# Performance work log

Measured on AMD Instinct MI355X. Metric: run time of the kernel, lower is better.

The kernel has to match this reference:

```python
import jax, jax.numpy as jnp
import numpy as np
import math

NQ = 12          # num_qubits
DEPTH = 4        # circuit_depth
DIM = 2 ** NQ    # state_dim = 4096
B = 4096         # batch

# CNOT ladder: (i,i+1) plus wrap-around (n-1,0) when n>2 (as in _init_circuit_parameters)
CNOT_PAIRS = [(i, i + 1) for i in range(NQ - 1)] + ([(NQ - 1, 0)] if NQ > 2 else [])


def _rx(theta):
    c = jnp.cos(theta / 2).astype(jnp.complex64)
    s = jnp.sin(theta / 2).astype(jnp.complex64) * (-1j)
    return jnp.stack([jnp.stack([c, s]), jnp.stack([s, c])])


def _ry(phi):
    c = jnp.cos(phi / 2).astype(jnp.complex64)
    s = jnp.sin(phi / 2).astype(jnp.complex64)
    return jnp.stack([jnp.stack([c, -s]), jnp.stack([s, c])])


def _rz(lam):
    lamc = lam.astype(jnp.complex64)
    e0 = jnp.exp(-1j * lamc / 2)
    e1 = jnp.exp(1j * lamc / 2)
    z = jnp.zeros((), jnp.complex64)
    return jnp.stack([jnp.stack([e0, z]), jnp.stack([z, e1])])


def _apply_1q(state, gate, q):
    # state: [B] + [2]*NQ, qubit q lives on axis q+1 (kron order: qubit 0 most significant)
    ax = q + 1
    s = jnp.moveaxis(state, ax, -1)
    s = jnp.einsum('ab,...b->...a', gate, s)
    return jnp.moveaxis(s, -1, ax)


def _apply_cnot(state, control, target):
    # flip target bit on the control=1 half of the state vector
    ac, at = control + 1, target + 1
    s0 = jnp.take(state, jnp.array([0]), axis=ac)
    s1 = jnp.take(state, jnp.array([1]), axis=ac)
    s1 = jnp.flip(s1, axis=at)
    return jnp.concatenate([s0, s1], axis=ac)


def setup_inputs() -> dict:
    key = jax.random.key(0)
    k1, k2, k3, k4 = jax.random.split(key, 4)
    return {
        'input_data': jax.random.normal(k1, (B, DIM), dtype=jnp.float32),
        'angles_x': jax.random.normal(k2, (DEPTH, NQ), dtype=jnp.float32) * 0.5,
        'angles_y': jax.random.normal(k3, (DEPTH, NQ), dtype=jnp.float32) * 0.5,
        'angles_z': jax.random.normal(k4, (DEPTH, NQ), dtype=jnp.float32) * 0.5,
    }


def reference(input_data, angles_x, angles_y, angles_z):
    # --- amplitude encoding (faithful to quantum_weight_memory) ---
    w = jnp.abs(input_data[:, :DIM])                      # [B, D]
    D = w.shape[1]
    s = jnp.sum(w, axis=1, keepdims=True)
    wn = jnp.where(s > 1e-8, w / jnp.sqrt(jnp.maximum(s, 1e-8)),
                   jnp.full_like(w, 1.0 / math.sqrt(D)))
    state = jnp.zeros((w.shape[0], DIM), jnp.complex64).at[:, 0].set(1.0)
    state = state.at[:, :D].set(wn.astype(jnp.complex64))
    norm = jnp.sqrt(jnp.sum(jnp.abs(state) ** 2, axis=1, keepdims=True))
    state = jnp.where(norm > 1e-8, state / jnp.maximum(norm, 1e-8), state)

    # --- parametrized circuit, applied as local state-vector updates ---
    state = state.reshape((state.shape[0],) + (2,) * NQ)
    for layer in range(DEPTH):
        for q in range(NQ):
            state = _apply_1q(state, _rx(angles_x[layer, q]), q)
            state = _apply_1q(state, _ry(angles_y[layer, q]), q)
            state = _apply_1q(state, _rz(angles_z[layer, q]), q)
        for c, t in CNOT_PAIRS:
            state = _apply_cnot(state, c, t)
    state = state.reshape(-1, DIM)

    # --- measurement ---
    probs = jnp.abs(state) ** 2
    return jnp.sqrt(probs[:, :DIM])
```

## Files before the change

### kernel.cpp

```cpp
#include <hip/hip_runtime.h>
#include <math.h>

#define DIM 4096

typedef _Float16 v8h __attribute__((ext_vector_type(8)));
typedef float v4f __attribute__((ext_vector_type(4)));

__device__ __forceinline__ int pinv(int s) {
  int p = __popc(s) & 1;
  int d = s ^ (p ? 0xC00 : 0);
  d ^= d >> 1; d ^= d >> 2; d ^= d >> 4; d ^= d >> 8;
  return d & 4095;
}
constexpr int pinv_c(int s) {
  int p = __builtin_popcount(s) & 1;
  int d = s ^ (p ? 0xC00 : 0);
  d ^= d >> 1; d ^= d >> 2; d ^= d >> 4; d ^= d >> 8;
  return d & 4095;
}

__device__ __forceinline__ int swz4(int row) {
  return (((row >> 1) ^ (row >> 5)) & 3) << 4;
}

constexpr int l0d(int d) {
  int row = (d & 15) * 16 + ((d >> 4) & 15);
  int f2 = ((row >> 1) ^ (row >> 5)) & 3;
  return (row << 6) ^ ((((d >> 8) & 15)) << 1) ^ (f2 << 4);
}

constexpr int DR1 = l0d(pinv_c(1 << 8));
constexpr int DR2 = l0d(pinv_c(2 << 8));
constexpr int DR3 = l0d(pinv_c(3 << 8));

template <int PASS>
__device__ __forceinline__ void do_pass(const char* src, char* dst,
                                        const v8h* __restrict__ Af, int mat, int t) {
  const int lane = t & 63, wv = t >> 6;
  const int m = lane & 15, q = lane >> 4, qb = q & 1, pm = q >> 1;
  const v8h b_re = Af[(mat * 2 + 0) * 64 + lane];
  const v8h b_im = Af[(mat * 2 + 1) * 64 + lane];
  int abase = 0;
  if constexpr (PASS == 2) {
    abase = l0d(pinv((q << 10) | (wv << 6) | m));
  }
#pragma unroll
  for (int tt = 0; tt < 4; ++tt) {
    const int t4 = wv * 4 + tt;
    const int row = t4 * 16 + m;
    const int sz = swz4(row);
    v8h a;
    if constexpr (PASS == 0) {
      a = *(const v8h*)(src + (((row << 6) + pm * 32 + qb * 16) ^ sz));
    } else {
      const int ad = ((row << 6) + qb * 32 + pm * 8) ^ sz;
      const uint2 lo = *(const uint2*)(src + ad);
      const uint2 hi = *(const uint2*)(src + (ad ^ 16));
      a = __builtin_bit_cast(v8h, make_uint4(lo.x, lo.y, hi.x, hi.y));
    }
    const v4f cre = __builtin_amdgcn_mfma_f32_16x16x32_f16(a, b_re, (v4f){0.f, 0.f, 0.f, 0.f}, 0, 0, 0);
    const v4f cim = __builtin_amdgcn_mfma_f32_16x16x32_f16(a, b_im, (v4f){0.f, 0.f, 0.f, 0.f}, 0, 0, 0);
    if constexpr (PASS < 2) {
      const int wrow = m * 16 + t4;
      v8h w;
#pragma unroll
      for (int r = 0; r < 4; ++r) {
        w[r] = (_Float16)cre[r];
        w[4 + r] = (_Float16)cim[r];
      }
      *(v8h*)(dst + (((wrow << 6) + q * 16) ^ swz4(wrow))) = w;
    } else {
      const int ab = abase ^ l0d(pinv_c(tt << 4));
      *(_Float16*)(dst + ab) = (_Float16)cre[0];
      *(_Float16*)(dst + (ab ^ DR1)) = (_Float16)cre[1];
      *(_Float16*)(dst + (ab ^ DR2)) = (_Float16)cre[2];
      *(_Float16*)(dst + (ab ^ DR3)) = (_Float16)cre[3];
      *(_Float16*)(dst + (ab ^ 32)) = (_Float16)cim[0];
      *(_Float16*)(dst + (ab ^ (DR1 ^ 32))) = (_Float16)cim[1];
      *(_Float16*)(dst + (ab ^ (DR2 ^ 32))) = (_Float16)cim[2];
      *(_Float16*)(dst + (ab ^ (DR3 ^ 32))) = (_Float16)cim[3];
    }
  }
}

__global__ void make_gates2(const float* __restrict__ ax, const float* __restrict__ ay,
                            const float* __restrict__ az, _Float16* __restrict__ Aw) {
  __shared__ float g4[48][4];
  const int id = threadIdx.x;
  if (id < 48) {
    float th = 0.5f * ax[id], ph = 0.5f * ay[id], lm = 0.5f * az[id];
    float c = cosf(th), s = sinf(th);
    float cy = cosf(ph), sy = sinf(ph);
    float cl = cosf(lm), sl = sinf(lm);
    float m00r = cy * c, m00i = sy * s;
    float m01r = -sy * c, m01i = -cy * s;
    g4[id][0] = cl * m00r + sl * m00i;
    g4[id][1] = cl * m00i - sl * m00r;
    g4[id][2] = cl * m01r + sl * m01i;
    g4[id][3] = cl * m01i - sl * m01r;
  }
  __syncthreads();
  const int mat = id >> 6, lane = id & 63;
  const int m = lane & 15, q = lane >> 4;
  const int layer = mat / 3, pass = mat % 3, qbase = pass * 4;
#pragma unroll
  for (int j = 0; j < 8; ++j) {
    const int k = q * 8 + j, kk = k & 15;
    float cr = 1.f, ci = 0.f;
#pragma unroll
    for (int bp = 3; bp >= 0; --bp) {
      const int qq = qbase + (3 - bp);
      const int ib = (m >> bp) & 1, kb = (kk >> bp) & 1;
      const float* gg = g4[layer * 12 + qq];
      float er, ei;
      if (ib == 0 && kb == 0) { er = gg[0]; ei = gg[1]; }
      else if (ib == 0 && kb == 1) { er = gg[2]; ei = gg[3]; }
      else if (ib == 1 && kb == 0) { er = -gg[2]; ei = gg[3]; }
      else { er = gg[0]; ei = -gg[1]; }
      const float nr = cr * er - ci * ei, ni = cr * ei + ci * er;
      cr = nr; ci = ni;
    }
    const float reval = (k < 16) ? cr : -ci;
    const float imval = (k < 16) ? ci : cr;
    Aw[((mat * 2 + 0) * 64 + lane) * 8 + j] = (_Float16)reval;
    Aw[((mat * 2 + 1) * 64 + lane) * 8 + j] = (_Float16)imval;
  }
}

__global__ __launch_bounds__(256, 4) void qsim3(const float* __restrict__ x,
                                                const v8h* __restrict__ Af,
                                                float* __restrict__ out) {
  __shared__ __align__(16) char buf[2][16384];
  const int t = threadIdx.x;
  const int b = blockIdx.x;
  const float* xb = x + (size_t)b * DIM;

  float w[16];
  float sw = 0.f, sw2 = 0.f;
#pragma unroll
  for (int j = 0; j < 16; ++j) {
    float a = fabsf(xb[t + (j << 8)]);
    w[j] = a; sw += a; sw2 += a * a;
  }
#pragma unroll
  for (int off = 32; off; off >>= 1) {
    sw += __shfl_down(sw, off, 64);
    sw2 += __shfl_down(sw2, off, 64);
  }
  float* red = (float*)buf[1];
  if ((t & 63) == 0) { red[t >> 6] = sw; red[4 + (t >> 6)] = sw2; }
  __syncthreads();
  sw = (red[0] + red[1]) + (red[2] + red[3]);
  sw2 = (red[4] + red[5]) + (red[6] + red[7]);

  float sc = 0.f;
  const bool ok = (sw > 1e-8f);
  if (ok) {
    float wnscale = rsqrtf(fmaxf(sw, 1e-8f));
    float norm = sqrtf(sw2 / sw);
    sc = ((norm > 1e-8f) ? (wnscale / fmaxf(norm, 1e-8f)) : wnscale) * 64.0f;
  }
  {
    const int row = ((t & 15) << 4) | (t >> 4);
    const int rb = (row << 6) ^ swz4(row);
    v8h h0, h1, z;
#pragma unroll
    for (int j = 0; j < 8; ++j) {
      h0[j] = (_Float16)(ok ? w[j] * sc : 1.0f);
      h1[j] = (_Float16)(ok ? w[8 + j] * sc : 1.0f);
      z[j] = (_Float16)0.f;
    }
    *(v8h*)(buf[0] + (rb ^ 0)) = h0;
    *(v8h*)(buf[0] + (rb ^ 16)) = h1;
    *(v8h*)(buf[0] + (rb ^ 32)) = z;
    *(v8h*)(buf[0] + (rb ^ 48)) = z;
  }
  __syncthreads();

  char* s = buf[0];
  char* d = buf[1];
#pragma unroll 1
  for (int l = 0; l < 4; ++l) {
    do_pass<0>(s, d, Af, l * 3 + 0, t);
    __syncthreads();
    do_pass<1>(d, s, Af, l * 3 + 1, t);
    __syncthreads();
    do_pass<2>(s, d, Af, l * 3 + 2, t);
    __syncthreads();
    char* tmp = s; s = d; d = tmp;
  }

  float* ob = out + (size_t)b * DIM;
  {
    const int row = ((t & 15) << 4) | (t >> 4);
    const int rb = (row << 6) ^ swz4(row);
    const v8h r0 = *(const v8h*)(s + (rb ^ 0));
    const v8h r1 = *(const v8h*)(s + (rb ^ 16));
    const v8h i0 = *(const v8h*)(s + (rb ^ 32));
    const v8h i1 = *(const v8h*)(s + (rb ^ 48));
#pragma unroll
    for (int j = 0; j < 8; ++j) {
      float re = (float)r0[j], im = (float)i0[j];
      ob[(j << 8) | t] = sqrtf(re * re + im * im) * 0.015625f;
      float re2 = (float)r1[j], im2 = (float)i1[j];
      ob[((j + 8) << 8) | t] = sqrtf(re2 * re2 + im2 * im2) * 0.015625f;
    }
  }
}

extern "C" void kernel_launch(void* const* d_in, const int* in_sizes, int n_in,
                              void* d_out, int out_size, void* d_ws, size_t ws_size,
                              hipStream_t stream) {
  const float* x = (const float*)d_in[0];
  const float* ax = (const float*)d_in[1];
  const float* ay = (const float*)d_in[2];
  const float* az = (const float*)d_in[3];
  _Float16* Aw = (_Float16*)d_ws;
  make_gates2<<<1, 768, 0, stream>>>(ax, ay, az, Aw);
  qsim3<<<4096, 256, 0, stream>>>(x, (const v8h*)Aw, (float*)d_out);
}
```

Measured before the change: 176.2 us.

## Replace scattered CNOT permutation stores with vectorized stores and fold permutation into loads

Pass 2 used to write eight scattered 2-byte halves per MFMA so that the CNOT-ladder permutation landed in the store addresses. It now writes two 8-byte vectors in plain order. The permutation is absorbed later, by Gray-code-style indexing plus byte perms in the next layer's first pass and in the final output read. Pass 1 loads become single 16-byte reads rearranged with permlane32_swap, and the LDS swizzle gains an extra bit to reduce bank conflicts. The aim is fewer LDS transactions and less address arithmetic, at the cost of more complex index logic with a higher risk of subtle permutation errors.

```diff
diff --git a/kernel.cpp b/kernel.cpp
--- a/kernel.cpp
+++ b/kernel.cpp
@@ -4,81 +4,76 @@
 #define DIM 4096
 
 typedef _Float16 v8h __attribute__((ext_vector_type(8)));
+typedef _Float16 v4h __attribute__((ext_vector_type(4)));
 typedef float v4f __attribute__((ext_vector_type(4)));
-
-__device__ __forceinline__ int pinv(int s) {
-  int p = __popc(s) & 1;
-  int d = s ^ (p ? 0xC00 : 0);
-  d ^= d >> 1; d ^= d >> 2; d ^= d >> 4; d ^= d >> 8;
-  return d & 4095;
-}
-constexpr int pinv_c(int s) {
-  int p = __builtin_popcount(s) & 1;
-  int d = s ^ (p ? 0xC00 : 0);
-  d ^= d >> 1; d ^= d >> 2; d ^= d >> 4; d ^= d >> 8;
-  return d & 4095;
-}
-
-__device__ __forceinline__ int swz4(int row) {
-  return (((row >> 1) ^ (row >> 5)) & 3) << 4;
-}
-
-constexpr int l0d(int d) {
-  int row = (d & 15) * 16 + ((d >> 4) & 15);
-  int f2 = ((row >> 1) ^ (row >> 5)) & 3;
-  return (row << 6) ^ ((((d >> 8) & 15)) << 1) ^ (f2 << 4);
-}
-
-constexpr int DR1 = l0d(pinv_c(1 << 8));
-constexpr int DR2 = l0d(pinv_c(2 << 8));
-constexpr int DR3 = l0d(pinv_c(3 << 8));
-
-template <int PASS>
-__device__ __forceinline__ void do_pass(const char* src, char* dst,
+typedef unsigned int v2u __attribute__((ext_vector_type(2)));
+
+__device__ __forceinline__ int adr(int row, int off) {
+  return ((row << 6) | off) ^ ((((row >> 1) ^ (row >> 5)) & 3) << 4)
+                            ^ (((row >> 4) & 1) << 6);
+}
+
+
+template <int PASS, bool FOLD>
+__device__ __forceinline__ void do_pass(const char* __restrict__ src, char* __restrict__ dst,
                                         const v8h* __restrict__ Af, int mat, int t) {
   const int lane = t & 63, wv = t >> 6;
-  const int m = lane & 15, q = lane >> 4, qb = q & 1, pm = q >> 1;
+  const int m = lane & 15, q = lane >> 4;
+  const int qb = q & 1, pm = q >> 1;
   const v8h b_re = Af[(mat * 2 + 0) * 64 + lane];
   const v8h b_im = Af[(mat * 2 + 1) * 64 + lane];
-  int abase = 0;
-  if constexpr (PASS == 2) {
-    abase = l0d(pinv((q << 10) | (wv << 6) | m));
-  }
+  const int gm = (m ^ (m >> 1)) & 15;
 #pragma unroll
   for (int tt = 0; tt < 4; ++tt) {
     const int t4 = wv * 4 + tt;
-    const int row = t4 * 16 + m;
-    const int sz = swz4(row);
     v8h a;
-    if constexpr (PASS == 0) {
-      a = *(const v8h*)(src + (((row << 6) + pm * 32 + qb * 16) ^ sz));
+    if constexpr (PASS == 0 && FOLD) {
+      const int t4g = t4 ^ (t4 >> 1);
+      const bool qs = ((qb ^ tt) & 1) != 0;
+      const int off = pm * 32 + (qs ? 16 : 0);
+      const int r0 = ((t4g ^ ((m & 1) << 3)) << 4) | gm;
+      const uint4 E = *(const uint4*)(src + adr(r0, off));
+      const uint4 O = *(const uint4*)(src + adr(r0 ^ 8, off));
+      const unsigned e0 = qs ? E.z : E.x, e1 = qs ? E.w : E.y;
+      const unsigned e2 = qs ? E.y : E.w, e3 = qs ? E.x : E.z;
+      const unsigned o0 = qs ? O.z : O.x, o1 = qs ? O.w : O.y;
+      const unsigned o2 = qs ? O.y : O.w, o3 = qs ? O.x : O.z;
+      uint4 av;
+      av.x = __builtin_amdgcn_perm(o0, e0, 0x07060100u);
+      av.y = __builtin_amdgcn_perm(o1, e1, 0x05040302u);
+      av.z = __builtin_amdgcn_perm(o2, e2, 0x07060100u);
+      av.w = __builtin_amdgcn_perm(o3, e3, 0x05040302u);
+      a = __builtin_bit_cast(v8h, av);
+    } else if constexpr (PASS == 0) {
+      a = *(const v8h*)(src + adr(t4 * 16 + m, pm * 32 + qb * 16));
     } else {
-      const int ad = ((row << 6) + qb * 32 + pm * 8) ^ sz;
-      const uint2 lo = *(const uint2*)(src + ad);
-      const uint2 hi = *(const uint2*)(src + (ad ^ 16));
-      a = __builtin_bit_cast(v8h, make_uint4(lo.x, lo.y, hi.x, hi.y));
+      const uint4 r = *(const uint4*)(src + adr(t4 * 16 + m, (2 * qb + pm) * 16));
+      const v2u s0 = __builtin_amdgcn_permlane32_swap(r.x, r.z, false, false);
+      const v2u s1 = __builtin_amdgcn_permlane32_swap(r.y, r.w, false, false);
+      uint4 av;
+      av.x = s0.x; av.y = s1.x; av.z = s0.y; av.w = s1.y;
+      a = __builtin_bit_cast(v8h, av);
     }
     const v4f cre = __builtin_amdgcn_mfma_f32_16x16x32_f16(a, b_re, (v4f){0.f, 0.f, 0.f, 0.f}, 0, 0, 0);
     const v4f cim = __builtin_amdgcn_mfma_f32_16x16x32_f16(a, b_im, (v4f){0.f, 0.f, 0.f, 0.f}, 0, 0, 0);
+    const int wrow = m * 16 + t4;
     if constexpr (PASS < 2) {
-      const int wrow = m * 16 + t4;
       v8h w;
 #pragma unroll
-      for (int r = 0; r < 4; ++r) {
-        w[r] = (_Float16)cre[r];
-        w[4 + r] = (_Float16)cim[r];
+      for (int r2 = 0; r2 < 4; ++r2) {
+        w[r2] = (_Float16)cre[r2];
+        w[4 + r2] = (_Float16)cim[r2];
       }
-      *(v8h*)(dst + (((wrow << 6) + q * 16) ^ swz4(wrow))) = w;
+      *(v8h*)(dst + adr(wrow, q * 16)) = w;
     } else {
-      const int ab = abase ^ l0d(pinv_c(tt << 4));
-      *(_Float16*)(dst + ab) = (_Float16)cre[0];
-      *(_Float16*)(dst + (ab ^ DR1)) = (_Float16)cre[1];
-      *(_Float16*)(dst + (ab ^ DR2)) = (_Float16)cre[2];
-      *(_Float16*)(dst + (ab ^ DR3)) = (_Float16)cre[3];
-      *(_Float16*)(dst + (ab ^ 32)) = (_Float16)cim[0];
-      *(_Float16*)(dst + (ab ^ (DR1 ^ 32))) = (_Float16)cim[1];
-      *(_Float16*)(dst + (ab ^ (DR2 ^ 32))) = (_Float16)cim[2];
-      *(_Float16*)(dst + (ab ^ (DR3 ^ 32))) = (_Float16)cim[3];
+      v4h wre, wim;
+#pragma unroll
+      for (int r2 = 0; r2 < 4; ++r2) {
+        wre[r2] = (_Float16)cre[r2];
+        wim[r2] = (_Float16)cim[r2];
+      }
+      *(v4h*)(dst + adr(wrow, q * 8)) = wre;
+      *(v4h*)(dst + adr(wrow, 32 + q * 8)) = wim;
     }
   }
 }
@@ -127,7 +122,7 @@
   }
 }
 
-__global__ __launch_bounds__(256, 4) void qsim3(const float* __restrict__ x,
+__global__ __launch_bounds__(256, 4) void qsim4(const float* __restrict__ x,
                                                 const v8h* __restrict__ Af,
                                                 float* __restrict__ out) {
   __shared__ __align__(16) char buf[2][16384];
@@ -139,8 +134,8 @@
   float sw = 0.f, sw2 = 0.f;
 #pragma unroll
   for (int j = 0; j < 16; ++j) {
-    float a = fabsf(xb[t + (j << 8)]);
-    w[j] = a; sw += a; sw2 += a * a;
+    float aa = fabsf(xb[t + (j << 8)]);
+    w[j] = aa; sw += aa; sw2 += aa * aa;
   }
 #pragma unroll
   for (int off = 32; off; off >>= 1) {
@@ -162,7 +157,6 @@
   }
   {
     const int row = ((t & 15) << 4) | (t >> 4);
-    const int rb = (row << 6) ^ swz4(row);
     v8h h0, h1, z;
 #pragma unroll
     for (int j = 0; j < 8; ++j) {
@@ -170,41 +164,60 @@
       h1[j] = (_Float16)(ok ? w[8 + j] * sc : 1.0f);
       z[j] = (_Float16)0.f;
     }
-    *(v8h*)(buf[0] + (rb ^ 0)) = h0;
-    *(v8h*)(buf[0] + (rb ^ 16)) = h1;
-    *(v8h*)(buf[0] + (rb ^ 32)) = z;
-    *(v8h*)(buf[0] + (rb ^ 48)) = z;
+    *(v8h*)(buf[0] + adr(row, 0)) = h0;
+    *(v8h*)(buf[0] + adr(row, 16)) = h1;
+    *(v8h*)(buf[0] + adr(row, 32)) = z;
+    *(v8h*)(buf[0] + adr(row, 48)) = z;
   }
   __syncthreads();
 
   char* s = buf[0];
   char* d = buf[1];
+  do_pass<0, false>(s, d, Af, 0, t); __syncthreads();
+  do_pass<1, false>(d, s, Af, 1, t); __syncthreads();
+  do_pass<2, false>(s, d, Af, 2, t); __syncthreads();
+  { char* tmp = s; s = d; d = tmp; }
 #pragma unroll 1
-  for (int l = 0; l < 4; ++l) {
-    do_pass<0>(s, d, Af, l * 3 + 0, t);
-    __syncthreads();
-    do_pass<1>(d, s, Af, l * 3 + 1, t);
-    __syncthreads();
-    do_pass<2>(s, d, Af, l * 3 + 2, t);
-    __syncthreads();
+  for (int l = 1; l < 4; ++l) {
+    do_pass<0, true>(s, d, Af, l * 3 + 0, t); __syncthreads();
+    do_pass<1, false>(d, s, Af, l * 3 + 1, t); __syncthreads();
+    do_pass<2, false>(s, d, Af, l * 3 + 2, t); __syncthreads();
     char* tmp = s; s = d; d = tmp;
   }
 
   float* ob = out + (size_t)b * DIM;
   {
-    const int row = ((t & 15) << 4) | (t >> 4);
-    const int rb = (row << 6) ^ swz4(row);
-    const v8h r0 = *(const v8h*)(s + (rb ^ 0));
-    const v8h r1 = *(const v8h*)(s + (rb ^ 16));
-    const v8h i0 = *(const v8h*)(s + (rb ^ 32));
-    const v8h i1 = *(const v8h*)(s + (rb ^ 48));
-#pragma unroll
-    for (int j = 0; j < 8; ++j) {
-      float re = (float)r0[j], im = (float)i0[j];
-      ob[(j << 8) | t] = sqrtf(re * re + im * im) * 0.015625f;
-      float re2 = (float)r1[j], im2 = (float)i1[j];
-      ob[((j + 8) << 8) | t] = sqrtf(re2 * re2 + im2 * im2) * 0.015625f;
-    }
+    const int g = t ^ (t >> 1);
+    const int re_row = (g & 15) * 16 + ((g >> 4) & 15);
+    const int ro = re_row ^ 8;
+    const int offA = (t & 1) ? 24 : 0;
+    const int offB = (t & 1) ? 16 : 8;
+    const v4h E0 = *(const v4h*)(s + adr(re_row, offA));
+    const v4h E1 = *(const v4h*)(s + adr(re_row, offB));
+    const v4h E2 = *(const v4h*)(s + adr(re_row, offA ^ 24));
+    const v4h E3 = *(const v4h*)(s + adr(re_row, offB ^ 24));
+    const v4h O0 = *(const v4h*)(s + adr(ro, offA));
+    const v4h O1 = *(const v4h*)(s + adr(ro, offB));
+    const v4h O2 = *(const v4h*)(s + adr(ro, offA ^ 24));
+    const v4h O3 = *(const v4h*)(s + adr(ro, offB ^ 24));
+    const v4h IE0 = *(const v4h*)(s + adr(re_row, 32 + offA));
+    const v4h IE1 = *(const v4h*)(s + adr(re_row, 32 + offB));
+    const v4h IE2 = *(const v4h*)(s + adr(re_row, 32 + (offA ^ 24)));
+    const v4h IE3 = *(const v4h*)(s + adr(re_row, 32 + (offB ^ 24)));
+    const v4h IO0 = *(const v4h*)(s + adr(ro, 32 + offA));
+    const v4h IO1 = *(const v4h*)(s + adr(ro, 32 + offB));
+    const v4h IO2 = *(const v4h*)(s + adr(ro, 32 + (offA ^ 24)));
+    const v4h IO3 = *(const v4h*)(s + adr(ro, 32 + (offB ^ 24)));
+#define MAG(J, VR, VI, IDX)                                           \
+  {                                                                   \
+    const float re_ = (float)VR[IDX], im_ = (float)VI[IDX];           \
+    ob[((J) << 8) | t] = sqrtf(re_ * re_ + im_ * im_) * 0.015625f;    \
+  }
+    MAG(0, E0, IE0, 0)  MAG(2, E0, IE0, 3)  MAG(4, E1, IE1, 2)  MAG(6, E1, IE1, 1)
+    MAG(8, E2, IE2, 0)  MAG(10, E2, IE2, 3) MAG(12, E3, IE3, 2) MAG(14, E3, IE3, 1)
+    MAG(1, O0, IO0, 1)  MAG(3, O0, IO0, 2)  MAG(5, O1, IO1, 3)  MAG(7, O1, IO1, 0)
+    MAG(9, O2, IO2, 1)  MAG(11, O2, IO2, 2) MAG(13, O3, IO3, 3) MAG(15, O3, IO3, 0)
+#undef MAG
   }
 }
 
@@ -217,5 +230,5 @@
   const float* az = (const float*)d_in[3];
   _Float16* Aw = (_Float16*)d_ws;
   make_gates2<<<1, 768, 0, stream>>>(ax, ay, az, Aw);
-  qsim3<<<4096, 256, 0, stream>>>(x, (const v8h*)Aw, (float*)d_out);
-}
+  qsim4<<<4096, 256, 0, stream>>>(x, (const v8h*)Aw, (float*)d_out);
+}
```

Result: faster. 159.0 us (-9.8%).
